# Kernel optimization log

Hardware: AMD Instinct MI355X
Metric: run time of the kernel (lower is better)

Reference implementation:

```python
import jax, jax.numpy as jnp
import numpy as np

N_CLASS = 32000
EMB = 1024
HID = 1024
BATCH = 256
SEQ = 256


def setup_inputs() -> dict:
    key = jax.random.key(0)
    ks = jax.random.split(key, 16)
    s = 0.02
    inp = {
        "X": jax.random.randint(ks[0], (BATCH, SEQ), 0, N_CLASS, dtype=jnp.int32),
        "C": jax.random.normal(ks[1], (N_CLASS, EMB), dtype=jnp.float32) * s,
    }
    gate_names = ["W_i1", "W_f1", "W_o1", "W_g1", "W_i2", "W_f2", "W_o2", "W_g2"]
    for i, n in enumerate(gate_names):
        inp[n] = jax.random.normal(ks[2 + i], (HID, EMB + HID), dtype=jnp.float32) * s
    # biases are initialized to ones in the original module
    for n in ["b_i1", "b_f1", "b_o1", "b_g1", "b_i2", "b_f2", "b_o2", "b_g2"]:
        inp[n] = jnp.ones((HID,), dtype=jnp.float32)
    inp["W_out"] = jax.random.normal(ks[10], (N_CLASS, HID), dtype=jnp.float32) * s
    inp["b_out"] = jnp.ones((N_CLASS,), dtype=jnp.float32)
    return inp


def _lstm_dir(Xt, Wi, bi, Wf, bf, Wo, bo, Wg, bg):
    """Run one LSTM direction over Xt: [T, B, E]. Returns final hidden [B, H]."""
    B = Xt.shape[1]
    H = bi.shape[0]
    h0 = jnp.zeros((B, H), Xt.dtype)
    c0 = jnp.zeros((B, H), Xt.dtype)

    def step(carry, x):
        h, c = carry
        xh = jnp.concatenate([x, h], axis=1)  # [B, E+H]
        i = jax.nn.sigmoid(xh @ Wi.T + bi)
        f = jax.nn.sigmoid(xh @ Wf.T + bf)
        o = jax.nn.sigmoid(xh @ Wo.T + bo)
        g = jnp.tanh(xh @ Wg.T + bg)
        c_new = f * c + i * g
        h_new = o * jnp.tanh(c_new)
        return (h_new, c_new), None

    (h, c), _ = jax.lax.scan(step, (h0, c0), Xt)
    return h


def reference(X, C, W_i1, W_f1, W_o1, W_g1, W_i2, W_f2, W_o2, W_g2,
              b_i1, b_f1, b_o1, b_g1, b_i2, b_f2, b_o2, b_g2, W_out, b_out):
    E = C[X]                       # [B, S, E] embedding lookup
    Xt = jnp.transpose(E, (1, 0, 2))  # [T, B, E]
    # forward direction
    h1 = _lstm_dir(Xt, W_i1, b_i1, W_f1, b_f1, W_o1, b_o1, W_g1, b_g1)
    # backward direction: original code detaches (numpy round-trip) before reversing
    Xr = jax.lax.stop_gradient(Xt)[::-1]
    h2 = _lstm_dir(Xr, W_i2, b_i2, W_f2, b_f2, W_o2, b_o2, W_g2, b_g2)
    return (h1 + h2) @ W_out.T + b_out  # [B, n_class]
```

## Files before the change

### kernel.cpp

```cpp
#include <hip/hip_runtime.h>
#include <hip/hip_bf16.h>
#include <stdint.h>
#include <math.h>

#define BATCH 256
#define SEQ   256
#define EMB   1024
#define HID   1024
#define NCLASS 32000
#define KTOT  2048
#define NGATE 8192

typedef __attribute__((ext_vector_type(8))) short bf16x8;
typedef __attribute__((ext_vector_type(4))) float f32x4;

__device__ __forceinline__ unsigned short f2b(float f) {
  union { float f; unsigned u; } v; v.f = f;
  unsigned r = v.u + 0x7FFFu + ((v.u >> 16) & 1u);
  return (unsigned short)(r >> 16);
}
__device__ __forceinline__ float b2f(unsigned short s) {
  union { unsigned u; float f; } v; v.u = ((unsigned)s) << 16;
  return v.f;
}
__device__ __forceinline__ void load_lds16(const void* g, void* l) {
  __builtin_amdgcn_global_load_lds(
      (const __attribute__((address_space(1))) unsigned int*)g,
      (__attribute__((address_space(3))) unsigned int*)l, 16, 0, 0);
}

__global__ void embed_kernel(const int* __restrict__ X, const float* __restrict__ C,
                             unsigned short* __restrict__ Xt) {
  int n = blockIdx.x;
  int t = n >> 8, b = n & 255;
  int tok = X[(size_t)b * SEQ + t];
  float4 v = ((const float4*)(C + (size_t)tok * EMB))[threadIdx.x];
  ushort4 o;
  o.x = f2b(v.x); o.y = f2b(v.y); o.z = f2b(v.z); o.w = f2b(v.w);
  ((ushort4*)(Xt + (size_t)n * EMB))[threadIdx.x] = o;
}

__global__ void castf_kernel(const float* __restrict__ src, unsigned short* __restrict__ dst,
                             int n4) {
  int i = blockIdx.x * blockDim.x + threadIdx.x;
  if (i < n4) {
    float4 v = ((const float4*)src)[i];
    ushort4 o;
    o.x = f2b(v.x); o.y = f2b(v.y); o.z = f2b(v.z); o.w = f2b(v.w);
    ((ushort4*)dst)[i] = o;
  }
}

__global__ void bcat_kernel(const float* b0, const float* b1, const float* b2,
                            const float* b3, const float* b4, const float* b5,
                            const float* b6, const float* b7, float* __restrict__ bcat) {
  int n = blockIdx.x * 256 + threadIdx.x;
  const float* bp[8] = {b0, b1, b2, b3, b4, b5, b6, b7};
  bcat[n] = bp[n >> 10][n & 1023];
}

__launch_bounds__(256)
__global__ void gx_gemm_kernel(const unsigned short* __restrict__ A,
                               const unsigned short* __restrict__ Bw,
                               const float* __restrict__ bcat,
                               unsigned short* __restrict__ Gx) {
  __shared__ unsigned short As[2][128][64];
  __shared__ unsigned short Bs[2][128][64];
  int bid = blockIdx.x;
  int m0 = (bid >> 6) * 128;
  int n0 = (bid & 63) * 128;
  int tid = threadIdx.x;

  auto stage = [&](int buf, int kb) {
    int kbase = kb * 64;
#pragma unroll
    for (int ri = 0; ri < 4; ++ri) {
      int slot = ri * 256 + tid;
      int row = slot >> 3;
      int ce  = (slot & 7) * 8;
      load_lds16(A + (size_t)(m0 + row) * EMB + kbase + ce, &As[buf][row][ce]);
    }
#pragma unroll
    for (int ri = 0; ri < 4; ++ri) {
      int slot = ri * 256 + tid;
      int row = slot >> 3;
      int ce  = (slot & 7) * 8;
      load_lds16(Bw + (size_t)(n0 + row) * KTOT + kbase + ce, &Bs[buf][row][ce]);
    }
  };

  int w = tid >> 6, lane = tid & 63;
  int lm = lane & 15, lq = lane >> 4;
  int wm = w & 1, wn = w >> 1;

  f32x4 zero = {0.f, 0.f, 0.f, 0.f};
  f32x4 acc[4][4];
#pragma unroll
  for (int mi = 0; mi < 4; ++mi)
#pragma unroll
    for (int ni = 0; ni < 4; ++ni) acc[mi][ni] = zero;

  stage(0, 0);
  for (int kb = 0; kb < 16; ++kb) {
    int cur = kb & 1;
    __syncthreads();
    if (kb + 1 < 16) stage(1 - cur, kb + 1);
#pragma unroll
    for (int kc = 0; kc < 2; ++kc) {
      bf16x8 af[4];
#pragma unroll
      for (int mi = 0; mi < 4; ++mi)
        af[mi] = *(const bf16x8*)&As[cur][wm * 64 + mi * 16 + lm][kc * 32 + lq * 8];
#pragma unroll
      for (int ni = 0; ni < 4; ++ni) {
        bf16x8 bb = *(const bf16x8*)&Bs[cur][wn * 64 + ni * 16 + lm][kc * 32 + lq * 8];
#pragma unroll
        for (int mi = 0; mi < 4; ++mi)
          acc[mi][ni] = __builtin_amdgcn_mfma_f32_16x16x32_bf16(af[mi], bb, acc[mi][ni], 0, 0, 0);
      }
    }
  }

#pragma unroll
  for (int ni = 0; ni < 4; ++ni) {
    int n = n0 + wn * 64 + ni * 16 + lm;
    float bn = bcat[n];
#pragma unroll
    for (int mi = 0; mi < 4; ++mi) {
#pragma unroll
      for (int reg = 0; reg < 4; ++reg) {
        int m = m0 + wm * 64 + mi * 16 + lq * 4 + reg;
        Gx[(size_t)m * NGATE + n] = f2b(acc[mi][ni][reg] + bn);
      }
    }
  }
}

#define BM 128
#define BN 64
#define BK 64
__launch_bounds__(256)
__global__ void lstm_step_kernel(const unsigned short* __restrict__ Xt,
                                 const unsigned short* __restrict__ Wcat,
                                 const unsigned short* __restrict__ Gx,
                                 const unsigned short* __restrict__ h_in,
                                 unsigned short* __restrict__ h_out,
                                 float* __restrict__ c_st,
                                 const float* __restrict__ b0, const float* __restrict__ b1,
                                 const float* __restrict__ b2, const float* __restrict__ b3,
                                 const float* __restrict__ b4, const float* __restrict__ b5,
                                 const float* __restrict__ b6, const float* __restrict__ b7,
                                 int t) {
  __shared__ unsigned short As[2][BM][BK];
  __shared__ unsigned short Bs[2][BN][BK];

  int bid = blockIdx.x;
  int d   = bid >> 7;
  int r   = bid & 127;
  int m0  = (r & 1) * BM;
  int j0  = (r >> 1) * 16;
  int td  = d ? (SEQ - 1 - t) : t;
  int tid = threadIdx.x;

  bool useGx = (Gx != nullptr);
  int  kiters = useGx ? (HID / BK) : (KTOT / BK);
  int  koff   = useGx ? EMB : 0;

  const unsigned short* Asrc0 = Xt  + ((size_t)td * BATCH + m0) * EMB;
  const unsigned short* Asrc1 = h_in + ((size_t)d * BATCH + m0) * HID;
  const unsigned short* Wd    = Wcat + (size_t)d * 4 * HID * KTOT;

  auto stageA = [&](int buf, int kb) {
    int kbase = kb * BK;
    const unsigned short* src; int ko;
    if (useGx)            { src = Asrc1; ko = kbase; }
    else if (kbase < EMB) { src = Asrc0; ko = kbase; }
    else                  { src = Asrc1; ko = kbase - EMB; }
#pragma unroll
    for (int ri = 0; ri < 4; ++ri) {
      int slot = ri * 256 + tid;
      int row = slot >> 3;
      int ce  = (slot & 7) * 8;
      load_lds16(src + (size_t)row * 1024 + ko + ce, &As[buf][row][ce]);
    }
  };
  auto stageB = [&](int buf, int kb) {
    int kbase = koff + kb * BK;
#pragma unroll
    for (int ri = 0; ri < 2; ++ri) {
      int slot = ri * 256 + tid;
      int rr  = slot >> 3;
      int g8  = rr >> 4;
      int jj  = rr & 15;
      int ce  = (slot & 7) * 8;
      load_lds16(Wd + (size_t)(g8 * HID + j0 + jj) * KTOT + kbase + ce, &Bs[buf][rr][ce]);
    }
  };

  int w = tid >> 6, lane = tid & 63;
  int lm = lane & 15, lq = lane >> 4;

  f32x4 zero = {0.f, 0.f, 0.f, 0.f};
  f32x4 acc[2][4];
#pragma unroll
  for (int mi = 0; mi < 2; ++mi)
#pragma unroll
    for (int g8 = 0; g8 < 4; ++g8) acc[mi][g8] = zero;

  stageA(0, 0); stageB(0, 0);
  for (int kb = 0; kb < kiters; ++kb) {
    int cur = kb & 1;
    __syncthreads();
    if (kb + 1 < kiters) { stageA(1 - cur, kb + 1); stageB(1 - cur, kb + 1); }
#pragma unroll
    for (int kc = 0; kc < 2; ++kc) {
      bf16x8 a0 = *(const bf16x8*)&As[cur][w * 32 +  0 + lm][kc * 32 + lq * 8];
      bf16x8 a1 = *(const bf16x8*)&As[cur][w * 32 + 16 + lm][kc * 32 + lq * 8];
#pragma unroll
      for (int g8 = 0; g8 < 4; ++g8) {
        bf16x8 bb = *(const bf16x8*)&Bs[cur][g8 * 16 + lm][kc * 32 + lq * 8];
        acc[0][g8] = __builtin_amdgcn_mfma_f32_16x16x32_bf16(a0, bb, acc[0][g8], 0, 0, 0);
        acc[1][g8] = __builtin_amdgcn_mfma_f32_16x16x32_bf16(a1, bb, acc[1][g8], 0, 0, 0);
      }
    }
  }

  const float* bi = d ? b4 : b0;
  const float* bf = d ? b5 : b1;
  const float* bo = d ? b6 : b2;
  const float* bgp= d ? b7 : b3;
  int j = j0 + lm;
  float vbi, vbf, vbo, vbg;
  if (!useGx) { vbi = bi[j]; vbf = bf[j]; vbo = bo[j]; vbg = bgp[j]; }
  else        { vbi = vbf = vbo = vbg = 0.f; }
  const unsigned short* gxb = nullptr;
  if (useGx)
    gxb = Gx + (size_t)td * BATCH * NGATE + (size_t)d * 4096 + j0 + lm;

#pragma unroll
  for (int mi = 0; mi < 2; ++mi) {
#pragma unroll
    for (int reg = 0; reg < 4; ++reg) {
      int b = m0 + w * 32 + mi * 16 + lq * 4 + reg;
      float pi = acc[mi][0][reg] + vbi;
      float pf = acc[mi][1][reg] + vbf;
      float po = acc[mi][2][reg] + vbo;
      float pg = acc[mi][3][reg] + vbg;
      if (useGx) {
        const unsigned short* g = gxb + (size_t)b * NGATE;
        pi += b2f(g[0]);
        pf += b2f(g[1024]);
        po += b2f(g[2048]);
        pg += b2f(g[3072]);
      }
      float ig = 1.f / (1.f + __expf(-pi));
      float fg = 1.f / (1.f + __expf(-pf));
      float og = 1.f / (1.f + __expf(-po));
      float gg = tanhf(pg);
      size_t ci = ((size_t)d * BATCH + b) * HID + j;
      float cn = fg * c_st[ci] + ig * gg;
      c_st[ci] = cn;
      h_out[ci] = f2b(og * tanhf(cn));
    }
  }
}

__global__ void hsum_kernel(const unsigned short* __restrict__ hfin,
                            unsigned short* __restrict__ hs) {
  int i = blockIdx.x * 256 + threadIdx.x;
  ushort4 a = ((const ushort4*)hfin)[i];
  ushort4 b = ((const ushort4*)(hfin + (size_t)BATCH * HID))[i];
  ushort4 o;
  o.x = f2b(b2f(a.x) + b2f(b.x));
  o.y = f2b(b2f(a.y) + b2f(b.y));
  o.z = f2b(b2f(a.z) + b2f(b.z));
  o.w = f2b(b2f(a.w) + b2f(b.w));
  ((ushort4*)hs)[i] = o;
}

__launch_bounds__(256)
__global__ void out_gemm_kernel(const unsigned short* __restrict__ A,
                                const unsigned short* __restrict__ B,
                                const float* __restrict__ bias,
                                float* __restrict__ Cout) {
  __shared__ unsigned short As[2][128][64];
  __shared__ unsigned short Bs[2][128][64];
  int bid = blockIdx.x;
  int m0 = (bid & 1) * 128;
  int n0 = (bid >> 1) * 128;
  int tid = threadIdx.x;

  auto stage = [&](int buf, int kb) {
    int kbase = kb * 64;
#pragma unroll
    for (int ri = 0; ri < 4; ++ri) {
      int slot = ri * 256 + tid;
      int row = slot >> 3;
      int ce  = (slot & 7) * 8;
      load_lds16(A + ((size_t)(m0 + row)) * HID + kbase + ce, &As[buf][row][ce]);
    }
#pragma unroll
    for (int ri = 0; ri < 4; ++ri) {
      int slot = ri * 256 + tid;
      int row = slot >> 3;
      int ce  = (slot & 7) * 8;
      load_lds16(B + ((size_t)(n0 + row)) * HID + kbase + ce, &Bs[buf][row][ce]);
    }
  };

  int w = tid >> 6, lane = tid & 63;
  int lm = lane & 15, lq = lane >> 4;
  int wm = w & 1, wn = w >> 1;

  f32x4 zero = {0.f, 0.f, 0.f, 0.f};
  f32x4 acc[4][4];
#pragma unroll
  for (int mi = 0; mi < 4; ++mi)
#pragma unroll
    for (int ni = 0; ni < 4; ++ni) acc[mi][ni] = zero;

  stage(0, 0);
  for (int kb = 0; kb < 16; ++kb) {
    int cur = kb & 1;
    __syncthreads();
    if (kb + 1 < 16) stage(1 - cur, kb + 1);
#pragma unroll
    for (int kc = 0; kc < 2; ++kc) {
      bf16x8 af[4];
#pragma unroll
      for (int mi = 0; mi < 4; ++mi)
        af[mi] = *(const bf16x8*)&As[cur][wm * 64 + mi * 16 + lm][kc * 32 + lq * 8];
#pragma unroll
      for (int ni = 0; ni < 4; ++ni) {
        bf16x8 bb = *(const bf16x8*)&Bs[cur][wn * 64 + ni * 16 + lm][kc * 32 + lq * 8];
#pragma unroll
        for (int mi = 0; mi < 4; ++mi)
          acc[mi][ni] = __builtin_amdgcn_mfma_f32_16x16x32_bf16(af[mi], bb, acc[mi][ni], 0, 0, 0);
      }
    }
  }

#pragma unroll
  for (int ni = 0; ni < 4; ++ni) {
    int n = n0 + wn * 64 + ni * 16 + lm;
    float bn = bias[n];
#pragma unroll
    for (int mi = 0; mi < 4; ++mi) {
#pragma unroll
      for (int reg = 0; reg < 4; ++reg) {
        int m = m0 + wm * 64 + mi * 16 + lq * 4 + reg;
        Cout[(size_t)m * NCLASS + n] = acc[mi][ni][reg] + bn;
      }
    }
  }
}

extern "C" void kernel_launch(void* const* d_in, const int* in_sizes, int n_in,
                              void* d_out, int out_size, void* d_ws, size_t ws_size,
                              hipStream_t stream) {
  const int*   X    = (const int*)d_in[0];
  const float* C    = (const float*)d_in[1];
  const float* Wg[8];
  for (int i = 0; i < 8; ++i) Wg[i] = (const float*)d_in[2 + i];
  const float* bg[8];
  for (int i = 0; i < 8; ++i) bg[i] = (const float*)d_in[10 + i];
  const float* Wout = (const float*)d_in[18];
  const float* bout = (const float*)d_in[19];
  float* out = (float*)d_out;

  const size_t szXt   = (size_t)SEQ * BATCH * EMB * 2;
  const size_t szWcat = (size_t)8 * HID * KTOT * 2;
  const size_t szWob  = (size_t)NCLASS * HID * 2;
  const size_t szH    = (size_t)2 * BATCH * HID * 2;
  const size_t szC    = (size_t)2 * BATCH * HID * 4;
  const size_t szHs   = (size_t)BATCH * HID * 2;
  const size_t szBc   = (size_t)NGATE * 4;
  const size_t szGx   = (size_t)SEQ * BATCH * NGATE * 2;

  uint8_t* p = (uint8_t*)d_ws;
  unsigned short* Xt   = (unsigned short*)p; p += szXt;
  unsigned short* Wcat = (unsigned short*)p; p += szWcat;
  unsigned short* Wob  = (unsigned short*)p; p += szWob;
  unsigned short* hb0  = (unsigned short*)p; p += szH;
  unsigned short* hb1  = (unsigned short*)p; p += szH;
  float*          cst  = (float*)p;          p += szC;
  unsigned short* hs   = (unsigned short*)p; p += szHs;
  float*          bcat = (float*)p;          p += szBc;
  unsigned short* Gx   = (unsigned short*)p; p += szGx;

  size_t need_full = (size_t)(p - (uint8_t*)d_ws);
  bool useGx = (ws_size >= need_full);
  if (!useGx) Gx = nullptr;

  hipMemsetAsync(hb0, 0, szH, stream);
  hipMemsetAsync(cst, 0, szC, stream);

  embed_kernel<<<SEQ * BATCH, 256, 0, stream>>>(X, C, Xt);
  for (int i = 0; i < 8; ++i)
    castf_kernel<<<2048, 256, 0, stream>>>(Wg[i], Wcat + (size_t)i * HID * KTOT,
                                           (HID * KTOT) / 4);
  castf_kernel<<<32000, 256, 0, stream>>>(Wout, Wob, (NCLASS * HID) / 4);

  if (useGx) {
    bcat_kernel<<<NGATE / 256, 256, 0, stream>>>(bg[0], bg[1], bg[2], bg[3],
                                                 bg[4], bg[5], bg[6], bg[7], bcat);
    gx_gemm_kernel<<<512 * 64, 256, 0, stream>>>(Xt, Wcat, bcat, Gx);
  }

  unsigned short* hbuf[2] = {hb0, hb1};
  for (int t = 0; t < SEQ; ++t) {
    lstm_step_kernel<<<256, 256, 0, stream>>>(
        Xt, Wcat, Gx, hbuf[t & 1], hbuf[(t + 1) & 1], cst,
        bg[0], bg[1], bg[2], bg[3], bg[4], bg[5], bg[6], bg[7], t);
  }
  hsum_kernel<<<256, 256, 0, stream>>>(hb0, hs);
  out_gemm_kernel<<<500, 256, 0, stream>>>(hs, Wob, bout, out);
}
```

Baseline: 10.51 ms.

## Replace per-step LSTM launches with a persistent cooperative kernel holding weights in LDS

Replaces the 256 per-timestep kernel launches with one cooperative persistent kernel. Each block keeps its 64x1024 slice of recurrent weights resident in LDS with an XOR swizzle, and keeps the cell state in registers. Timesteps are separated by a global atomic-counter grid barrier. This removes launch overhead and the repeated reload of recurrent weights every step, in exchange for a spin barrier and a single-block-per-CU occupancy requirement (128KB LDS for weights). The per-step kernel is kept only as a fallback when the workspace cannot hold Gx.

```diff
diff --git a/kernel.cpp b/kernel.cpp
--- a/kernel.cpp
+++ b/kernel.cpp
@@ -136,13 +136,141 @@
   }
 }
 
+__launch_bounds__(256, 1)
+__global__ void lstm_persist_kernel(const unsigned short* __restrict__ Gx,
+                                    const unsigned short* __restrict__ Wcat,
+                                    unsigned short* __restrict__ hb0,
+                                    unsigned short* __restrict__ hb1,
+                                    unsigned int* __restrict__ bar) {
+  __shared__ unsigned short Wlds[64 * 1024];
+  __shared__ unsigned short As[2][128 * 64];
+
+  int bid = blockIdx.x;
+  int d   = bid >> 7;
+  int r   = bid & 127;
+  int m0  = (r & 1) * 128;
+  int j0  = (r >> 1) * 16;
+  int tid = threadIdx.x;
+  int w = tid >> 6, lane = tid & 63;
+  int lm = lane & 15, lq = lane >> 4;
+
+  const unsigned short* Wd = Wcat + (size_t)d * 4 * HID * KTOT;
+
+#pragma unroll
+  for (int riw = 0; riw < 32; ++riw) {
+    int s   = riw * 256 + tid;
+    int row = s >> 7;
+    int blk = s & 127;
+    int gblk = blk ^ (row & 7);
+    int g8 = row >> 4, jj = row & 15;
+    load_lds16(Wd + (size_t)(g8 * HID + j0 + jj) * KTOT + EMB + gblk * 8,
+               &Wlds[row * 1024 + blk * 8]);
+  }
+  __syncthreads();
+
+  float c_reg[2][4];
+#pragma unroll
+  for (int mi = 0; mi < 2; ++mi)
+#pragma unroll
+    for (int rg = 0; rg < 4; ++rg) c_reg[mi][rg] = 0.f;
+
+  unsigned short* hb[2] = {hb0, hb1};
+  int j = j0 + lm;
+
+  for (int t = 0; t < SEQ; ++t) {
+    int td = d ? (SEQ - 1 - t) : t;
+    const unsigned short* hin = hb[t & 1] + ((size_t)d * BATCH + m0) * HID;
+    unsigned short* hout = hb[(t + 1) & 1];
+
+    const unsigned short* gxb =
+        Gx + ((size_t)td * BATCH) * NGATE + (size_t)d * 4096 + (size_t)(j0 + lm);
+    unsigned short gxr[2][4][4];
+#pragma unroll
+    for (int mi = 0; mi < 2; ++mi)
+#pragma unroll
+      for (int rg = 0; rg < 4; ++rg) {
+        int b = m0 + w * 32 + mi * 16 + lq * 4 + rg;
+        const unsigned short* gp = gxb + (size_t)b * NGATE;
+#pragma unroll
+        for (int g8 = 0; g8 < 4; ++g8) gxr[mi][rg][g8] = gp[g8 * 1024];
+      }
+
+    auto stageA = [&](int buf, int kb) {
+      int kbase = kb * 64;
+#pragma unroll
+      for (int ri = 0; ri < 4; ++ri) {
+        int s   = ri * 256 + tid;
+        int row = s >> 3;
+        int c   = s & 7;
+        int gc  = c ^ (row & 7);
+        load_lds16(hin + (size_t)row * HID + kbase + gc * 8, &As[buf][s * 8]);
+      }
+    };
+
+    f32x4 zero = {0.f, 0.f, 0.f, 0.f};
+    f32x4 acc[2][4];
+#pragma unroll
+    for (int mi = 0; mi < 2; ++mi)
+#pragma unroll
+      for (int g8 = 0; g8 < 4; ++g8) acc[mi][g8] = zero;
+
+    stageA(0, 0);
+    for (int kb = 0; kb < 16; ++kb) {
+      int cur = kb & 1;
+      __syncthreads();
+      if (kb + 1 < 16) stageA(1 - cur, kb + 1);
+#pragma unroll
+      for (int kc = 0; kc < 2; ++kc) {
+        int sw = ((kc * 4 + lq) ^ (lm & 7)) * 8;
+        bf16x8 a0 = *(const bf16x8*)&As[cur][(w * 32 +  0 + lm) * 64 + sw];
+        bf16x8 a1 = *(const bf16x8*)&As[cur][(w * 32 + 16 + lm) * 64 + sw];
+#pragma unroll
+        for (int g8 = 0; g8 < 4; ++g8) {
+          bf16x8 bb = *(const bf16x8*)&Wlds[(g8 * 16 + lm) * 1024 + kb * 64 + sw];
+          acc[0][g8] = __builtin_amdgcn_mfma_f32_16x16x32_bf16(a0, bb, acc[0][g8], 0, 0, 0);
+          acc[1][g8] = __builtin_amdgcn_mfma_f32_16x16x32_bf16(a1, bb, acc[1][g8], 0, 0, 0);
+        }
+      }
+    }
+
+#pragma unroll
+    for (int mi = 0; mi < 2; ++mi) {
+#pragma unroll
+      for (int rg = 0; rg < 4; ++rg) {
+        int b = m0 + w * 32 + mi * 16 + lq * 4 + rg;
+        float pi = acc[mi][0][rg] + b2f(gxr[mi][rg][0]);
+        float pf = acc[mi][1][rg] + b2f(gxr[mi][rg][1]);
+        float po = acc[mi][2][rg] + b2f(gxr[mi][rg][2]);
+        float pg = acc[mi][3][rg] + b2f(gxr[mi][rg][3]);
+        float ig = 1.f / (1.f + __expf(-pi));
+        float fg = 1.f / (1.f + __expf(-pf));
+        float og = 1.f / (1.f + __expf(-po));
+        float gg = tanhf(pg);
+        float cn = fg * c_reg[mi][rg] + ig * gg;
+        c_reg[mi][rg] = cn;
+        hout[((size_t)d * BATCH + b) * HID + j] = f2b(og * tanhf(cn));
+      }
+    }
+
+    __syncthreads();
+    if (tid == 0) {
+      __threadfence();
+      atomicAdd(bar, 1u);
+      unsigned target = (unsigned)(t + 1) * gridDim.x;
+      while (__hip_atomic_load(bar, __ATOMIC_RELAXED, __HIP_MEMORY_SCOPE_AGENT) < target)
+        __builtin_amdgcn_s_sleep(2);
+      __threadfence();
+    }
+    __syncthreads();
+  }
+}
+
 #define BM 128
 #define BN 64
 #define BK 64
 __launch_bounds__(256)
 __global__ void lstm_step_kernel(const unsigned short* __restrict__ Xt,
                                  const unsigned short* __restrict__ Wcat,
-                                 const unsigned short* __restrict__ Gx,
                                  const unsigned short* __restrict__ h_in,
                                  unsigned short* __restrict__ h_out,
                                  float* __restrict__ c_st,
@@ -153,7 +281,6 @@
                                  int t) {
   __shared__ unsigned short As[2][BM][BK];
   __shared__ unsigned short Bs[2][BN][BK];
-
   int bid = blockIdx.x;
   int d   = bid >> 7;
   int r   = bid & 127;
@@ -162,10 +289,6 @@
   int td  = d ? (SEQ - 1 - t) : t;
   int tid = threadIdx.x;
 
-  bool useGx = (Gx != nullptr);
-  int  kiters = useGx ? (HID / BK) : (KTOT / BK);
-  int  koff   = useGx ? EMB : 0;
-
   const unsigned short* Asrc0 = Xt  + ((size_t)td * BATCH + m0) * EMB;
   const unsigned short* Asrc1 = h_in + ((size_t)d * BATCH + m0) * HID;
   const unsigned short* Wd    = Wcat + (size_t)d * 4 * HID * KTOT;
@@ -173,9 +296,7 @@
   auto stageA = [&](int buf, int kb) {
     int kbase = kb * BK;
     const unsigned short* src; int ko;
-    if (useGx)            { src = Asrc1; ko = kbase; }
-    else if (kbase < EMB) { src = Asrc0; ko = kbase; }
-    else                  { src = Asrc1; ko = kbase - EMB; }
+    if (kbase < EMB) { src = Asrc0; ko = kbase; } else { src = Asrc1; ko = kbase - EMB; }
 #pragma unroll
     for (int ri = 0; ri < 4; ++ri) {
       int slot = ri * 256 + tid;
@@ -185,7 +306,7 @@
     }
   };
   auto stageB = [&](int buf, int kb) {
-    int kbase = koff + kb * BK;
+    int kbase = kb * BK;
 #pragma unroll
     for (int ri = 0; ri < 2; ++ri) {
       int slot = ri * 256 + tid;
@@ -208,10 +329,10 @@
     for (int g8 = 0; g8 < 4; ++g8) acc[mi][g8] = zero;
 
   stageA(0, 0); stageB(0, 0);
-  for (int kb = 0; kb < kiters; ++kb) {
+  for (int kb = 0; kb < KTOT / BK; ++kb) {
     int cur = kb & 1;
     __syncthreads();
-    if (kb + 1 < kiters) { stageA(1 - cur, kb + 1); stageB(1 - cur, kb + 1); }
+    if (kb + 1 < KTOT / BK) { stageA(1 - cur, kb + 1); stageB(1 - cur, kb + 1); }
 #pragma unroll
     for (int kc = 0; kc < 2; ++kc) {
       bf16x8 a0 = *(const bf16x8*)&As[cur][w * 32 +  0 + lm][kc * 32 + lq * 8];
@@ -230,13 +351,7 @@
   const float* bo = d ? b6 : b2;
   const float* bgp= d ? b7 : b3;
   int j = j0 + lm;
-  float vbi, vbf, vbo, vbg;
-  if (!useGx) { vbi = bi[j]; vbf = bf[j]; vbo = bo[j]; vbg = bgp[j]; }
-  else        { vbi = vbf = vbo = vbg = 0.f; }
-  const unsigned short* gxb = nullptr;
-  if (useGx)
-    gxb = Gx + (size_t)td * BATCH * NGATE + (size_t)d * 4096 + j0 + lm;
-
+  float vbi = bi[j], vbf = bf[j], vbo = bo[j], vbg = bgp[j];
 #pragma unroll
   for (int mi = 0; mi < 2; ++mi) {
 #pragma unroll
@@ -246,13 +361,6 @@
       float pf = acc[mi][1][reg] + vbf;
       float po = acc[mi][2][reg] + vbo;
       float pg = acc[mi][3][reg] + vbg;
-      if (useGx) {
-        const unsigned short* g = gxb + (size_t)b * NGATE;
-        pi += b2f(g[0]);
-        pf += b2f(g[1024]);
-        po += b2f(g[2048]);
-        pg += b2f(g[3072]);
-      }
       float ig = 1.f / (1.f + __expf(-pi));
       float fg = 1.f / (1.f + __expf(-pf));
       float og = 1.f / (1.f + __expf(-po));
@@ -375,6 +483,7 @@
   const size_t szC    = (size_t)2 * BATCH * HID * 4;
   const size_t szHs   = (size_t)BATCH * HID * 2;
   const size_t szBc   = (size_t)NGATE * 4;
+  const size_t szBar  = 256;
   const size_t szGx   = (size_t)SEQ * BATCH * NGATE * 2;
 
   uint8_t* p = (uint8_t*)d_ws;
@@ -386,14 +495,14 @@
   float*          cst  = (float*)p;          p += szC;
   unsigned short* hs   = (unsigned short*)p; p += szHs;
   float*          bcat = (float*)p;          p += szBc;
+  unsigned int*   bar  = (unsigned int*)p;   p += szBar;
   unsigned short* Gx   = (unsigned short*)p; p += szGx;
 
   size_t need_full = (size_t)(p - (uint8_t*)d_ws);
   bool useGx = (ws_size >= need_full);
-  if (!useGx) Gx = nullptr;
 
   hipMemsetAsync(hb0, 0, szH, stream);
-  hipMemsetAsync(cst, 0, szC, stream);
+  hipMemsetAsync(bar, 0, 4, stream);
 
   embed_kernel<<<SEQ * BATCH, 256, 0, stream>>>(X, C, Xt);
   for (int i = 0; i < 8; ++i)
@@ -405,14 +514,20 @@
     bcat_kernel<<<NGATE / 256, 256, 0, stream>>>(bg[0], bg[1], bg[2], bg[3],
                                                  bg[4], bg[5], bg[6], bg[7], bcat);
     gx_gemm_kernel<<<512 * 64, 256, 0, stream>>>(Xt, Wcat, bcat, Gx);
-  }
-
-  unsigned short* hbuf[2] = {hb0, hb1};
-  for (int t = 0; t < SEQ; ++t) {
-    lstm_step_kernel<<<256, 256, 0, stream>>>(
-        Xt, Wcat, Gx, hbuf[t & 1], hbuf[(t + 1) & 1], cst,
-        bg[0], bg[1], bg[2], bg[3], bg[4], bg[5], bg[6], bg[7], t);
-  }
+
+    void* args[] = {(void*)&Gx, (void*)&Wcat, (void*)&hb0, (void*)&hb1, (void*)&bar};
+    hipLaunchCooperativeKernel(lstm_persist_kernel, dim3(256), dim3(256),
+                               args, 0, stream);
+  } else {
+    hipMemsetAsync(cst, 0, szC, stream);
+    unsigned short* hbuf[2] = {hb0, hb1};
+    for (int t = 0; t < SEQ; ++t) {
+      lstm_step_kernel<<<256, 256, 0, stream>>>(
+          Xt, Wcat, hbuf[t & 1], hbuf[(t + 1) & 1], cst,
+          bg[0], bg[1], bg[2], bg[3], bg[4], bg[5], bg[6], bg[7], t);
+    }
+  }
+
   hsum_kernel<<<256, 256, 0, stream>>>(hb0, hs);
   out_gemm_kernel<<<500, 256, 0, stream>>>(hs, Wob, bout, out);
 }
```

Measured after the change: 12.54 ms. +19.4%, slower.
